# Kernel tuning notes

Measured on AMD Instinct MI355X. Metric: run time of the kernel, lower is better.

## Reference

```python
import jax, jax.numpy as jnp
import numpy as np
import math

M = 0.5
S = 64.0
COS_M = math.cos(M)
SIN_M = math.sin(M)
MIN_COS = math.cos(math.pi - M)
NUM_CLASSES = 100000


def _l2norm(x, eps=1e-12):
    # matches F.normalize: x / max(||x||, eps)
    n = jnp.sqrt(jnp.sum(x * x, axis=-1, keepdims=True))
    return x / jnp.maximum(n, eps)


def setup_inputs() -> dict:
    key = jax.random.key(0)
    k1, k2, k3 = jax.random.split(key, 3)
    feats = jax.random.normal(k1, (8, 128, 512), dtype=jnp.float32)
    w = jax.random.normal(k2, (NUM_CLASSES, 512), dtype=jnp.float32)
    labels = jax.random.randint(k3, (1024,), 0, NUM_CLASSES, dtype=jnp.int32)
    return {"feats": feats, "w": w, "labels": labels}


def reference(feats, w, labels):
    d = feats.shape[-1]
    f = _l2norm(feats).reshape(-1, d)          # [N, d]
    wn = _l2norm(w)                            # [C, d]
    cos_theta = jnp.clip(jnp.einsum('nd,cd->nc', f, wn), -1.0, 1.0)  # [N, C]
    sin_theta = jnp.sqrt(1.0 - cos_theta * cos_theta + 1e-5)
    cos_theta_m = cos_theta * COS_M - sin_theta * SIN_M
    target_logit = jnp.where(cos_theta > MIN_COS, cos_theta_m,
                             cos_theta - sin_theta * M)
    # apply margin only at the label column
    onehot = jax.nn.one_hot(labels, cos_theta.shape[1], dtype=cos_theta.dtype)
    logits = (onehot * target_logit + (1.0 - onehot) * cos_theta) * S
    logp = jax.nn.log_softmax(logits, axis=-1)
    nll = -jnp.take_along_axis(logp, labels[:, None].astype(jnp.int32), axis=1)[:, 0]
    return jnp.mean(nll)
```

## Files before the change

kernel.cpp:

```cpp
#include <hip/hip_runtime.h>
#include <hip/hip_bf16.h>
#include <stdint.h>

#define NUM_CLASSES 100000
#define C_PAD       100096
#define NROWS       1024
#define KDIM        512
#define BM          128
#define BN          128
#define BK          32

#define L2E64 92.3324826f

typedef __bf16 bf16x8 __attribute__((ext_vector_type(8)));
typedef float  f32x4  __attribute__((ext_vector_type(4)));
typedef unsigned short u16x8 __attribute__((ext_vector_type(8)));

__device__ __forceinline__ unsigned short f2bf(float x) {
    unsigned int u = __float_as_uint(x);
    u = u + 0x7fffu + ((u >> 16) & 1u);
    return (unsigned short)(u >> 16);
}
__device__ __forceinline__ float bf2f(unsigned short x) {
    return __uint_as_float(((unsigned int)x) << 16);
}
__device__ __forceinline__ float fexp64(float c) {
    return exp2f(fmaf(c, L2E64, -L2E64));
}
__device__ __forceinline__ void gload_lds16(const void* g, void* l) {
    __builtin_amdgcn_global_load_lds(
        (const __attribute__((address_space(1))) unsigned int*)g,
        (__attribute__((address_space(3))) unsigned int*)l,
        16, 0, 0);
}

__global__ void norm_rows_bf16(const float* __restrict__ in,
                               unsigned short* __restrict__ out,
                               int rows_valid, int rows_total) {
    const int lane = threadIdx.x & 63;
    const int row  = blockIdx.x * 4 + (threadIdx.x >> 6);
    if (row >= rows_total) return;
    unsigned short* dst = out + (size_t)row * KDIM + lane * 8;
    if (row >= rows_valid) {
        u16x8 z;
        #pragma unroll
        for (int i = 0; i < 8; ++i) z[i] = 0;
        *(u16x8*)dst = z;
        return;
    }
    const float4* p = (const float4*)(in + (size_t)row * KDIM + lane * 8);
    float4 a = p[0], b = p[1];
    float ss = a.x*a.x + a.y*a.y + a.z*a.z + a.w*a.w
             + b.x*b.x + b.y*b.y + b.z*b.z + b.w*b.w;
    #pragma unroll
    for (int m = 1; m < 64; m <<= 1) ss += __shfl_xor(ss, m, 64);
    float scale = 1.0f / fmaxf(sqrtf(ss), 1e-12f);
    float v[8] = {a.x, a.y, a.z, a.w, b.x, b.y, b.z, b.w};
    u16x8 o;
    #pragma unroll
    for (int i = 0; i < 8; ++i) o[i] = f2bf(v[i] * scale);
    *(u16x8*)dst = o;
}

__global__ __launch_bounds__(256) void arcface_gemm(
        const unsigned short* __restrict__ fb,
        const unsigned short* __restrict__ wb,
        float* __restrict__ rowsum) {
    __shared__ __align__(16) unsigned short ldsA[BM * BK];
    __shared__ __align__(16) unsigned short ldsB[BN * BK];
    __shared__ float lds_rs[BM];

    const int tid  = threadIdx.x;
    const int lane = tid & 63;
    const int wid  = tid >> 6;
    const int wr   = wid >> 1;
    const int wc   = wid & 1;
    const int row0 = blockIdx.y * BM;
    const int col0 = blockIdx.x * BN;
    const int l15  = lane & 15;
    const int kg   = lane >> 4;

    f32x4 acc[4][4];
    #pragma unroll
    for (int m = 0; m < 4; ++m)
        #pragma unroll
        for (int n = 0; n < 4; ++n)
            #pragma unroll
            for (int j = 0; j < 4; ++j) acc[m][n][j] = 0.f;

    const char* fbB = (const char*)fb;
    const char* wbB = (const char*)wb;
    const int o0 = tid * 16;

    for (int kt = 0; kt < KDIM / BK; ++kt) {
        __syncthreads();
        const int kb = kt * (BK * 2);
        #pragma unroll
        for (int c = 0; c < 2; ++c) {
            const int o  = o0 + c * 4096;
            const int r  = o >> 6;
            const int cb = o & 63;
            gload_lds16(fbB + (size_t)(row0 + r) * (KDIM * 2) + kb + cb,
                        (char*)ldsA + o);
            gload_lds16(wbB + (size_t)(col0 + r) * (KDIM * 2) + kb + cb,
                        (char*)ldsB + o);
        }
        __syncthreads();

        bf16x8 af[4], bfr[4];
        #pragma unroll
        for (int m = 0; m < 4; ++m) {
            const int rr = wr * 64 + m * 16 + l15;
            af[m] = *(const bf16x8*)((const char*)ldsA + rr * 64 + kg * 16);
        }
        #pragma unroll
        for (int n = 0; n < 4; ++n) {
            const int cr = wc * 64 + n * 16 + l15;
            bfr[n] = *(const bf16x8*)((const char*)ldsB + cr * 64 + kg * 16);
        }
        #pragma unroll
        for (int m = 0; m < 4; ++m)
            #pragma unroll
            for (int n = 0; n < 4; ++n)
                acc[m][n] = __builtin_amdgcn_mfma_f32_16x16x32_bf16(
                                af[m], bfr[n], acc[m][n], 0, 0, 0);
    }

    if (tid < BM) lds_rs[tid] = 0.f;
    __syncthreads();

    float rs[4][4];
    #pragma unroll
    for (int m = 0; m < 4; ++m)
        #pragma unroll
        for (int j = 0; j < 4; ++j) rs[m][j] = 0.f;

    #pragma unroll
    for (int n = 0; n < 4; ++n) {
        const int colg = col0 + wc * 64 + n * 16 + l15;
        const bool valid = colg < NUM_CLASSES;
        #pragma unroll
        for (int m = 0; m < 4; ++m) {
            #pragma unroll
            for (int j = 0; j < 4; ++j) {
                float c = acc[m][n][j];
                c = fminf(fmaxf(c, -1.f), 1.f);
                float t = fexp64(c);
                rs[m][j] += valid ? t : 0.f;
            }
        }
    }
    #pragma unroll
    for (int m = 0; m < 4; ++m) {
        #pragma unroll
        for (int j = 0; j < 4; ++j) {
            float v = rs[m][j];
            v += __shfl_xor(v, 1, 64);
            v += __shfl_xor(v, 2, 64);
            v += __shfl_xor(v, 4, 64);
            v += __shfl_xor(v, 8, 64);
            rs[m][j] = v;
        }
    }
    if (l15 == 0) {
        #pragma unroll
        for (int m = 0; m < 4; ++m)
            #pragma unroll
            for (int j = 0; j < 4; ++j)
                atomicAdd(&lds_rs[wr * 64 + m * 16 + kg * 4 + j], rs[m][j]);
    }
    __syncthreads();
    if (tid < BM) atomicAdd(&rowsum[row0 + tid], lds_rs[tid]);
}

__global__ void label_dot(const unsigned short* __restrict__ fb,
                          const unsigned short* __restrict__ wb,
                          const int* __restrict__ labels,
                          float* __restrict__ coslab) {
    const int lane = threadIdx.x & 63;
    const int row  = blockIdx.x * 4 + (threadIdx.x >> 6);
    if (row >= NROWS) return;
    const int lab = labels[row];
    u16x8 a = *(const u16x8*)(fb + (size_t)row * KDIM + lane * 8);
    u16x8 b = *(const u16x8*)(wb + (size_t)lab * KDIM + lane * 8);
    float s = 0.f;
    #pragma unroll
    for (int i = 0; i < 8; ++i) s = fmaf(bf2f(a[i]), bf2f(b[i]), s);
    #pragma unroll
    for (int m = 1; m < 64; m <<= 1) s += __shfl_xor(s, m, 64);
    if (lane == 0) coslab[row] = s;
}

__global__ void finalize(const float* __restrict__ rowsum,
                         const float* __restrict__ coslab,
                         float* __restrict__ out) {
    const float COS_M   =  0.87758256189f;
    const float SIN_M   =  0.47942553860f;
    const float MIN_COS = -0.87758256189f;
    __shared__ float red[256];
    const int tid = threadIdx.x;
    float acc = 0.f;
    for (int r = tid; r < NROWS; r += 256) {
        float c = fminf(fmaxf(coslab[r], -1.f), 1.f);
        float sn = sqrtf(1.f - c * c + 1e-5f);
        float cm = c * COS_M - sn * SIN_M;
        float target = (c > MIN_COS) ? cm : (c - sn * 0.5f);
        float adj = rowsum[r] - fexp64(c) + fexp64(target);
        acc += 64.f + logf(adj) - 64.f * target;
    }
    red[tid] = acc;
    __syncthreads();
    for (int s = 128; s > 0; s >>= 1) {
        if (tid < s) red[tid] += red[tid + s];
        __syncthreads();
    }
    if (tid == 0) out[0] = red[0] / (float)NROWS;
}

extern "C" void kernel_launch(void* const* d_in, const int* in_sizes, int n_in,
                              void* d_out, int out_size, void* d_ws, size_t ws_size,
                              hipStream_t stream) {
    const float* feats  = (const float*)d_in[0];
    const float* w      = (const float*)d_in[1];
    const int*   labels = (const int*)d_in[2];
    float* out = (float*)d_out;

    char* ws = (char*)d_ws;
    unsigned short* wb = (unsigned short*)ws;
    unsigned short* fb = (unsigned short*)(ws + (size_t)C_PAD * KDIM * 2);
    float* rowsum = (float*)(ws + (size_t)C_PAD * KDIM * 2
                                + (size_t)NROWS * KDIM * 2);
    float* coslab = rowsum + NROWS;

    hipMemsetAsync(rowsum, 0, NROWS * sizeof(float), stream);
    norm_rows_bf16<<<C_PAD / 4, 256, 0, stream>>>(w, wb, NUM_CLASSES, C_PAD);
    norm_rows_bf16<<<NROWS / 4, 256, 0, stream>>>(feats, fb, NROWS, NROWS);
    dim3 grid(C_PAD / BN, NROWS / BM);
    arcface_gemm<<<grid, 256, 0, stream>>>(fb, wb, rowsum);
    label_dot<<<NROWS / 4, 256, 0, stream>>>(fb, wb, labels, coslab);
    finalize<<<1, 256, 0, stream>>>(rowsum, coslab, out);
}
```

Measured before the change: 481.0 us.

## Pre-tile bf16 operands into k-major blocks and remap workgroups for L2 reuse

The normalization kernels now write bf16 rows into a blocked layout in which each 128-row block stores its K-tiles contiguously, k-group-major. GEMM tile loads become contiguous 8KB copies, and LDS reads use a kg*2048 + row*16 layout that avoids the 64-byte row stride bank conflicts. The grid is flattened to 1D and remapped so that the 8 row blocks sharing a weight column tile run close together, which should improve L2 reuse of W. This adds index complexity to the normalization and label_dot kernels, and the remap formula hardcodes the grid size.

```diff
diff --git a/kernel.cpp b/kernel.cpp
--- a/kernel.cpp
+++ b/kernel.cpp
@@ -9,6 +9,10 @@
 #define BM          128
 #define BN          128
 #define BK          32
+#define NKT         (KDIM / BK)
+#define TILE_BYTES  8192
+#define RB_BYTES    (NKT * TILE_BYTES)
+#define RB_U16      (RB_BYTES / 2)
 
 #define L2E64 92.3324826f
 
@@ -34,13 +38,16 @@
         16, 0, 0);
 }
 
-__global__ void norm_rows_bf16(const float* __restrict__ in,
-                               unsigned short* __restrict__ out,
-                               int rows_valid, int rows_total) {
+
+__global__ void norm_rows_tiled(const float* __restrict__ in,
+                                unsigned short* __restrict__ out,
+                                int rows_valid, int rows_total) {
     const int lane = threadIdx.x & 63;
     const int row  = blockIdx.x * 4 + (threadIdx.x >> 6);
     if (row >= rows_total) return;
-    unsigned short* dst = out + (size_t)row * KDIM + lane * 8;
+    unsigned short* dst = out + (size_t)(row >> 7) * RB_U16
+                              + (lane >> 2) * 4096 + (lane & 3) * 1024
+                              + (row & 127) * 8;
     if (row >= rows_valid) {
         u16x8 z;
         #pragma unroll
@@ -63,8 +70,8 @@
 }
 
 __global__ __launch_bounds__(256) void arcface_gemm(
-        const unsigned short* __restrict__ fb,
-        const unsigned short* __restrict__ wb,
+        const unsigned short* __restrict__ fbT,
+        const unsigned short* __restrict__ wbT,
         float* __restrict__ rowsum) {
     __shared__ __align__(16) unsigned short ldsA[BM * BK];
     __shared__ __align__(16) unsigned short ldsB[BN * BK];
@@ -75,11 +82,18 @@
     const int wid  = tid >> 6;
     const int wr   = wid >> 1;
     const int wc   = wid & 1;
-    const int row0 = blockIdx.y * BM;
-    const int col0 = blockIdx.x * BN;
     const int l15  = lane & 15;
     const int kg   = lane >> 4;
 
+    const int wgid = (blockIdx.x & 7) * 782 + (blockIdx.x >> 3);
+    const int colb = wgid >> 3;
+    const int mrow = wgid & 7;
+    const int row0 = mrow * BM;
+    const int col0 = colb * BN;
+
+    const char* aBase = (const char*)fbT + (size_t)mrow * RB_BYTES;
+    const char* bBase = (const char*)wbT + (size_t)colb * RB_BYTES;
+
     f32x4 acc[4][4];
     #pragma unroll
     for (int m = 0; m < 4; ++m)
@@ -88,22 +102,17 @@
             #pragma unroll
             for (int j = 0; j < 4; ++j) acc[m][n][j] = 0.f;
 
-    const char* fbB = (const char*)fb;
-    const char* wbB = (const char*)wb;
     const int o0 = tid * 16;
 
-    for (int kt = 0; kt < KDIM / BK; ++kt) {
+    for (int kt = 0; kt < NKT; ++kt) {
         __syncthreads();
-        const int kb = kt * (BK * 2);
+        const char* aT = aBase + kt * TILE_BYTES;
+        const char* bT = bBase + kt * TILE_BYTES;
         #pragma unroll
         for (int c = 0; c < 2; ++c) {
-            const int o  = o0 + c * 4096;
-            const int r  = o >> 6;
-            const int cb = o & 63;
-            gload_lds16(fbB + (size_t)(row0 + r) * (KDIM * 2) + kb + cb,
-                        (char*)ldsA + o);
-            gload_lds16(wbB + (size_t)(col0 + r) * (KDIM * 2) + kb + cb,
-                        (char*)ldsB + o);
+            const int o = o0 + c * 4096;
+            gload_lds16(aT + o, (char*)ldsA + o);
+            gload_lds16(bT + o, (char*)ldsB + o);
         }
         __syncthreads();
 
@@ -111,12 +120,12 @@
         #pragma unroll
         for (int m = 0; m < 4; ++m) {
             const int rr = wr * 64 + m * 16 + l15;
-            af[m] = *(const bf16x8*)((const char*)ldsA + rr * 64 + kg * 16);
+            af[m] = *(const bf16x8*)((const char*)ldsA + kg * 2048 + rr * 16);
         }
         #pragma unroll
         for (int n = 0; n < 4; ++n) {
             const int cr = wc * 64 + n * 16 + l15;
-            bfr[n] = *(const bf16x8*)((const char*)ldsB + cr * 64 + kg * 16);
+            bfr[n] = *(const bf16x8*)((const char*)ldsB + kg * 2048 + cr * 16);
         }
         #pragma unroll
         for (int m = 0; m < 4; ++m)
@@ -173,16 +182,20 @@
     if (tid < BM) atomicAdd(&rowsum[row0 + tid], lds_rs[tid]);
 }
 
-__global__ void label_dot(const unsigned short* __restrict__ fb,
-                          const unsigned short* __restrict__ wb,
+__global__ void label_dot(const unsigned short* __restrict__ fbT,
+                          const unsigned short* __restrict__ wbT,
                           const int* __restrict__ labels,
                           float* __restrict__ coslab) {
     const int lane = threadIdx.x & 63;
     const int row  = blockIdx.x * 4 + (threadIdx.x >> 6);
     if (row >= NROWS) return;
     const int lab = labels[row];
-    u16x8 a = *(const u16x8*)(fb + (size_t)row * KDIM + lane * 8);
-    u16x8 b = *(const u16x8*)(wb + (size_t)lab * KDIM + lane * 8);
+    const size_t fo = (size_t)(row >> 7) * RB_U16 + (lane >> 2) * 4096
+                    + (lane & 3) * 1024 + (row & 127) * 8;
+    const size_t wo = (size_t)(lab >> 7) * RB_U16 + (lane >> 2) * 4096
+                    + (lane & 3) * 1024 + (lab & 127) * 8;
+    u16x8 a = *(const u16x8*)(fbT + fo);
+    u16x8 b = *(const u16x8*)(wbT + wo);
     float s = 0.f;
     #pragma unroll
     for (int i = 0; i < 8; ++i) s = fmaf(bf2f(a[i]), bf2f(b[i]), s);
@@ -226,17 +239,16 @@
     float* out = (float*)d_out;
 
     char* ws = (char*)d_ws;
-    unsigned short* wb = (unsigned short*)ws;
-    unsigned short* fb = (unsigned short*)(ws + (size_t)C_PAD * KDIM * 2);
+    unsigned short* wbT = (unsigned short*)ws;
+    unsigned short* fbT = (unsigned short*)(ws + (size_t)C_PAD * KDIM * 2);
     float* rowsum = (float*)(ws + (size_t)C_PAD * KDIM * 2
                                 + (size_t)NROWS * KDIM * 2);
     float* coslab = rowsum + NROWS;
 
     hipMemsetAsync(rowsum, 0, NROWS * sizeof(float), stream);
-    norm_rows_bf16<<<C_PAD / 4, 256, 0, stream>>>(w, wb, NUM_CLASSES, C_PAD);
-    norm_rows_bf16<<<NROWS / 4, 256, 0, stream>>>(feats, fb, NROWS, NROWS);
-    dim3 grid(C_PAD / BN, NROWS / BM);
-    arcface_gemm<<<grid, 256, 0, stream>>>(fb, wb, rowsum);
-    label_dot<<<NROWS / 4, 256, 0, stream>>>(fb, wb, labels, coslab);
+    norm_rows_tiled<<<C_PAD / 4, 256, 0, stream>>>(w, wbT, NUM_CLASSES, C_PAD);
+    norm_rows_tiled<<<NROWS / 4, 256, 0, stream>>>(feats, fbT, NROWS, NROWS);
+    arcface_gemm<<<(C_PAD / BN) * (NROWS / BM), 256, 0, stream>>>(fbT, wbT, rowsum);
+    label_dot<<<NROWS / 4, 256, 0, stream>>>(fbT, wbT, labels, coslab);
     finalize<<<1, 256, 0, stream>>>(rowsum, coslab, out);
 }
```

Measured after the change: 475.7 us. No clear change (-1.1%).
